# Kernel optimization log

Hardware: AMD Instinct MI355X
Metric: run time of the kernel (lower is better)

The kernel has to match this reference:

```python
import jax, jax.numpy as jnp
import numpy as np

B, CIN, CNECK, COUT = 8, 128, 128, 256
NV, NF = 10242, 20480  # icosphere level 5: nv = 10*4^5+2, nf = 20*4^5
EPS = 1e-5


def spmatmul(x, rows, cols, vals, m):
    # x: [..., N]; out[..., r] += vals[k] * x[..., cols[k]] for rows[k] == r
    g = x[..., cols] * vals
    return jnp.zeros(x.shape[:-1] + (m,), x.dtype).at[..., rows].add(g)


def conv1x1(x, w, b):
    # x: [B, Cin, N], w: [Cout, Cin], b: [Cout]
    return jnp.einsum('oi,bin->bon', w, x) + b[None, :, None]


def batchnorm1d(x, gamma, beta):
    # training-mode BN over (batch, spatial) per channel, biased variance
    mean = jnp.mean(x, axis=(0, 2), keepdims=True)
    var = jnp.var(x, axis=(0, 2), keepdims=True)
    xhat = (x - mean) * jax.lax.rsqrt(var + EPS)
    return gamma[None, :, None] * xhat + beta[None, :, None]


def setup_inputs() -> dict:
    key = jax.random.key(0)
    ks = jax.random.split(key, 16)

    def coo(k, nrows, per_row, ncols, scale):
        rows = jnp.repeat(jnp.arange(nrows, dtype=jnp.int32), per_row)
        cols = jax.random.randint(k, (nrows * per_row,), 0, ncols, dtype=jnp.int32)
        vals = jax.random.normal(jax.random.fold_in(k, 1), (nrows * per_row,), jnp.float32) * scale
        return rows, cols, vals

    Gr, Gc, Gv = coo(ks[0], 3 * NF, 3, NV, 0.5)
    Lr, Lc, Lv = coo(ks[1], NV, 7, NV, 0.3)
    Fr, Fc, Fv = coo(ks[2], NV, 6, NF, 1.0 / 6.0)

    def nrm(k, shape, scale=1.0):
        return jax.random.normal(k, shape, jnp.float32) * scale

    s_in = 1.0 / np.sqrt(CIN)
    s_nk = 1.0 / np.sqrt(CNECK)
    s_cf = 1.0 / np.sqrt(4 * CNECK)
    return {
        'x': nrm(ks[3], (B, CIN, NV)),
        'w1a': nrm(ks[4], (CNECK, CIN), s_in), 'b1a': nrm(ks[5], (CNECK,), s_in),
        'g1a': jnp.ones((CNECK,), jnp.float32), 'be1a': jnp.zeros((CNECK,), jnp.float32),
        'coeffs': nrm(ks[6], (CNECK * 4, CNECK), s_cf),
        'g2a': jnp.ones((CNECK,), jnp.float32), 'be2a': jnp.zeros((CNECK,), jnp.float32),
        'w3a': nrm(ks[7], (COUT, CNECK), s_nk), 'b3a': nrm(ks[8], (COUT,), s_nk),
        'g3a': jnp.ones((COUT,), jnp.float32), 'be3a': jnp.zeros((COUT,), jnp.float32),
        'w1b': nrm(ks[9], (COUT, CIN), s_in), 'b1b': nrm(ks[10], (COUT,), s_in),
        'g1b': jnp.ones((COUT,), jnp.float32), 'be1b': jnp.zeros((COUT,), jnp.float32),
        'G_vals': Gv, 'L_vals': Lv, 'F2V_vals': Fv,
        'EW': nrm(ks[11], (NF, 3)), 'NS': nrm(ks[12], (NF, 3)),
        'G_rows': Gr, 'G_cols': Gc,
        'L_rows': Lr, 'L_cols': Lc,
        'F2V_rows': Fr, 'F2V_cols': Fc,
    }


def mesh_conv(h, coeffs, G_rows, G_cols, G_vals, L_rows, L_cols, L_vals,
              F2V_rows, F2V_cols, F2V_vals, EW, NS):
    b, c, nv = h.shape
    # gradient on faces: [B,C,3*NF] -> [B,C,3,NF] -> [B,C,NF,3]
    grad_face = spmatmul(h, G_rows, G_cols, G_vals, 3 * NF)
    grad_face = grad_face.reshape(b, c, 3, NF).transpose(0, 1, 3, 2)
    laplacian = spmatmul(h, L_rows, L_cols, L_vals, NV)
    identity = h  # stride=1 => nv_prev == nv
    gf_ew = jnp.sum(grad_face * EW, axis=-1)  # [B,C,NF]
    gf_ns = jnp.sum(grad_face * NS, axis=-1)
    gv_ew = spmatmul(gf_ew, F2V_rows, F2V_cols, F2V_vals, NV)
    gv_ns = spmatmul(gf_ns, F2V_rows, F2V_cols, F2V_vals, NV)
    feat = jnp.stack([identity, laplacian, gv_ew, gv_ns], axis=-1)  # [B,C,NV,4]
    # [B,NV,C*4] @ [C*4,Cout] -> [B,Cout,NV]  (note: no bias added in original forward)
    out = jnp.matmul(feat.transpose(0, 2, 1, 3).reshape(b, nv, c * 4), coeffs)
    return out.transpose(0, 2, 1)


def reference(x, w1a, b1a, g1a, be1a, coeffs, g2a, be2a, w3a, b3a, g3a, be3a,
              w1b, b1b, g1b, be1b, G_vals, L_vals, F2V_vals, EW, NS,
              G_rows, G_cols, L_rows, L_cols, F2V_rows, F2V_cols):
    # shortcut branch: conv_1b -> bn_1b
    x2 = batchnorm1d(conv1x1(x, w1b, b1b), g1b, be1b)
    # main branch
    h = jax.nn.relu(batchnorm1d(conv1x1(x, w1a, b1a), g1a, be1a))
    h = mesh_conv(h, coeffs, G_rows, G_cols, G_vals, L_rows, L_cols, L_vals,
                  F2V_rows, F2V_cols, F2V_vals, EW, NS)
    h = jax.nn.relu(batchnorm1d(h, g2a, be2a))
    x1 = batchnorm1d(conv1x1(h, w3a, b3a), g3a, be3a)
    return jax.nn.relu(x1 + x2)
```

## Files before the change

### kernel.cpp

```cpp
#include <hip/hip_runtime.h>
#include <math.h>

#define BB   8
#define NVV  10242
#define NFF  20480
#define EPSBN 1e-5f
#define GRAM_BLOCKS 644

typedef __attribute__((ext_vector_type(8))) short bf16x8_t;
typedef __attribute__((ext_vector_type(4))) float f32x4_t;

__device__ inline float bf2f(ushort u) {
    union { uint i; float f; } v; v.i = ((uint)u) << 16; return v.f;
}
__device__ inline ushort f2bf(float f) {
    union { float f; uint i; } v; v.f = f;
    const uint r = v.i + 0x7fffu + ((v.i >> 16) & 1u);
    return (ushort)(r >> 16);
}
__device__ inline void unpack2(uint w, float& lo, float& hi) {
    union { uint i; float f; } a, b;
    a.i = w << 16; b.i = w & 0xffff0000u;
    lo = a.f; hi = b.f;
}
__device__ inline uint pack2(float lo, float hi) {
    return (uint)f2bf(lo) | ((uint)f2bf(hi) << 16);
}
__device__ inline void fma8(const uint4 hv, const float w, float s[8]) {
    float lo, hi;
    unpack2(hv.x, lo, hi); s[0] = fmaf(w, lo, s[0]); s[1] = fmaf(w, hi, s[1]);
    unpack2(hv.y, lo, hi); s[2] = fmaf(w, lo, s[2]); s[3] = fmaf(w, hi, s[3]);
    unpack2(hv.z, lo, hi); s[4] = fmaf(w, lo, s[4]); s[5] = fmaf(w, hi, s[5]);
    unpack2(hv.w, lo, hi); s[6] = fmaf(w, lo, s[6]); s[7] = fmaf(w, hi, s[7]);
}
__device__ inline uint4 pack8(const float s[8]) {
    uint4 p;
    p.x = pack2(s[0], s[1]); p.y = pack2(s[2], s[3]);
    p.z = pack2(s[4], s[5]); p.w = pack2(s[6], s[7]);
    return p;
}

__global__ __launch_bounds__(256)
void gram_kernel(const float* __restrict__ x, float* __restrict__ gramPart,
                 float* __restrict__ xsumPart, uint* __restrict__ xTu)
{
    __shared__ __align__(16) ushort Ahi[128 * 64];
    __shared__ __align__(16) ushort Alo[128 * 64];
    const int t = threadIdx.x;
    const int l = t & 63, wid = t >> 6;
    const int l15 = l & 15, l4 = l >> 4;
    f32x4_t acc[2][8];
#pragma unroll
    for (int m = 0; m < 2; ++m)
#pragma unroll
        for (int n = 0; n < 8; ++n) acc[m][n] = (f32x4_t){0.f, 0.f, 0.f, 0.f};
    float xs[8] = {0.f, 0.f, 0.f, 0.f, 0.f, 0.f, 0.f, 0.f};

    for (int s = 0; s < 2; ++s) {
        const int cc = blockIdx.x * 2 + s;
        const int b = cc / 161, tb = cc % 161, v0 = tb * 64;
#pragma unroll
        for (int i = 0; i < 8; ++i) {
            const int item = t + (i << 8);
            const int c = item >> 4, vq = item & 15;
            const int gv = v0 + (vq << 2);
            const float* xp = x + ((size_t)b * 128 + c) * NVV + gv;
            float4 xv = make_float4(0.f, 0.f, 0.f, 0.f);
            if (gv + 4 <= NVV) {
                xv = *reinterpret_cast<const float4*>(xp);
            } else {
                if (gv     < NVV) xv.x = xp[0];
                if (gv + 1 < NVV) xv.y = xp[1];
            }
            xs[i] += xv.x + xv.y + xv.z + xv.w;
            const ushort h0 = f2bf(xv.x), h1 = f2bf(xv.y), h2 = f2bf(xv.z), h3 = f2bf(xv.w);
            const ushort e0 = f2bf(xv.x - bf2f(h0)), e1 = f2bf(xv.y - bf2f(h1));
            const ushort e2 = f2bf(xv.z - bf2f(h2)), e3 = f2bf(xv.w - bf2f(h3));
            uint2 hp, lp;
            hp.x = (uint)h0 | ((uint)h1 << 16); hp.y = (uint)h2 | ((uint)h3 << 16);
            lp.x = (uint)e0 | ((uint)e1 << 16); lp.y = (uint)e2 | ((uint)e3 << 16);
            const int byte = (c << 7) + (vq << 3);
            const int swz = byte ^ ((c & 7) << 4);
            *reinterpret_cast<uint2*>((char*)Ahi + swz) = hp;
            *reinterpret_cast<uint2*>((char*)Alo + swz) = lp;
        }
        __syncthreads();
        {
            const int v = t & 63, cq = t >> 6;
            const int gv = v0 + v;
            if (gv < NVV) {
                uint4* rowp = reinterpret_cast<uint4*>(xTu + ((size_t)b * NVV + gv) * 64) + (cq << 2);
#pragma unroll
                for (int k2 = 0; k2 < 4; ++k2) {
                    uint wrd[4];
#pragma unroll
                    for (int w2 = 0; w2 < 4; ++w2) {
                        const int c0 = (cq << 5) + (k2 << 3) + (w2 << 1);
                        const int b0 = ((c0) << 7) + (v << 1);
                        const int b1 = ((c0 + 1) << 7) + (v << 1);
                        const ushort q0 = *reinterpret_cast<const ushort*>((const char*)Ahi + (b0 ^ ((c0 & 7) << 4)));
                        const ushort q1 = *reinterpret_cast<const ushort*>((const char*)Ahi + (b1 ^ (((c0 + 1) & 7) << 4)));
                        wrd[w2] = (uint)q0 | ((uint)q1 << 16);
                    }
                    rowp[k2] = make_uint4(wrd[0], wrd[1], wrd[2], wrd[3]);
                }
            }
        }
#pragma unroll
        for (int kk2 = 0; kk2 < 2; ++kk2) {
            bf16x8_t ah[2], al[2];
#pragma unroll
            for (int m = 0; m < 2; ++m) {
                const int row = wid * 32 + m * 16 + l15;
                const int byte = (row << 7) + (kk2 << 6) + (l4 << 4);
                ah[m] = *reinterpret_cast<const bf16x8_t*>((const char*)Ahi + (byte ^ ((row & 7) << 4)));
                al[m] = *reinterpret_cast<const bf16x8_t*>((const char*)Alo + (byte ^ ((row & 7) << 4)));
            }
#pragma unroll
            for (int n = 0; n < 8; ++n) {
                const int rn = n * 16 + l15;
                const int byte = (rn << 7) + (kk2 << 6) + (l4 << 4);
                const bf16x8_t bh = *reinterpret_cast<const bf16x8_t*>((const char*)Ahi + (byte ^ ((rn & 7) << 4)));
                const bf16x8_t bl = *reinterpret_cast<const bf16x8_t*>((const char*)Alo + (byte ^ ((rn & 7) << 4)));
#pragma unroll
                for (int m = 0; m < 2; ++m) {
                    acc[m][n] = __builtin_amdgcn_mfma_f32_16x16x32_bf16(ah[m], bh, acc[m][n], 0, 0, 0);
                    acc[m][n] = __builtin_amdgcn_mfma_f32_16x16x32_bf16(ah[m], bl, acc[m][n], 0, 0, 0);
                    acc[m][n] = __builtin_amdgcn_mfma_f32_16x16x32_bf16(al[m], bh, acc[m][n], 0, 0, 0);
                }
            }
        }
        __syncthreads();
    }
    float* gp = gramPart + (size_t)blockIdx.x * 16384;
#pragma unroll
    for (int m = 0; m < 2; ++m)
#pragma unroll
        for (int n = 0; n < 8; ++n)
#pragma unroll
            for (int j = 0; j < 4; ++j) {
                const int row = wid * 32 + m * 16 + l4 * 4 + j;
                const int col = n * 16 + l15;
                gp[row * 128 + col] = acc[m][n][j];
            }
#pragma unroll
    for (int i = 0; i < 8; ++i) {
        xs[i] += __shfl_xor(xs[i], 1);
        xs[i] += __shfl_xor(xs[i], 2);
        xs[i] += __shfl_xor(xs[i], 4);
        xs[i] += __shfl_xor(xs[i], 8);
    }
    if ((l & 15) == 0) {
#pragma unroll
        for (int i = 0; i < 8; ++i)
            xsumPart[(size_t)blockIdx.x * 128 + wid * 4 + l4 + i * 16] = xs[i];
    }
}

__global__ void reduce_gram_kernel(const float* __restrict__ gp, const float* __restrict__ xp,
                                   float* __restrict__ Gram, float* __restrict__ xsum)
{
    const int tid = blockIdx.x * 256 + threadIdx.x;
    for (int e = tid; e < 16384; e += 64 * 256) {
        float s = 0.f;
        for (int i = 0; i < GRAM_BLOCKS; ++i) s += gp[(size_t)i * 16384 + e];
        Gram[e] = s;
    }
    if (blockIdx.x == 0 && threadIdx.x < 128) {
        float s = 0.f;
        for (int i = 0; i < GRAM_BLOCKS; ++i) s += xp[(size_t)i * 128 + threadIdx.x];
        xsum[threadIdx.x] = s;
    }
}

__global__ __launch_bounds__(128)
void stats_ab_kernel(const float* __restrict__ Gram, const float* __restrict__ xsum,
                     const float* __restrict__ w1a, const float* __restrict__ g1a,
                     const float* __restrict__ be1a,
                     const float* __restrict__ w1b, const float* __restrict__ g1b,
                     const float* __restrict__ be1b,
                     float* __restrict__ alpha_a, float* __restrict__ beta_a,
                     float* __restrict__ alpha_b, float* __restrict__ beta_b)
{
    const int t = threadIdx.x;
    const int cc = blockIdx.x;
    const float invN = 1.f / (float)(BB * NVV);
    const bool isA = cc < 128;
    const int c = isA ? cc : cc - 128;
    const float* Wrow = isA ? (w1a + (size_t)c * 128) : (w1b + (size_t)c * 128);
    __shared__ float Wr[128];
    __shared__ float red[4];
    Wr[t] = Wrow[t];
    __syncthreads();
    float gi = 0.f;
    const float* Grow = Gram + (size_t)t * 128;
    for (int j = 0; j < 128; ++j) gi = fmaf(Grow[j], Wr[j], gi);
    float pi = Wr[t] * gi * invN;
    float qi = (xsum[t] * invN) * Wr[t];
    for (int off = 32; off > 0; off >>= 1) {
        pi += __shfl_down(pi, off);
        qi += __shfl_down(qi, off);
    }
    const int wid = t >> 6;
    if ((t & 63) == 0) { red[wid] = pi; red[2 + wid] = qi; }
    __syncthreads();
    if (t == 0) {
        const float P = red[0] + red[1], Q = red[2] + red[3];
        const float var = P - Q * Q;
        const float g = isA ? g1a[c] : g1b[c];
        const float be = isA ? be1a[c] : be1b[c];
        const float a = g * rsqrtf(var + EPSBN);
        if (isA) { alpha_a[c] = a; beta_a[c] = be - a * Q; }
        else     { alpha_b[c] = a; beta_b[c] = be - a * Q; }
    }
}

__global__ __launch_bounds__(256)
void prepack_weights_kernel(const float* __restrict__ w1a, const float* __restrict__ w1b,
                            const float* __restrict__ w3a, uint* __restrict__ wpk)
{
    const int j = blockIdx.x * 256 + threadIdx.x;
    const int seg = j >> 12;
    const int slab = seg >> 1, kc = (seg & 1) << 6;
    const int u = j & 4095;
    const int o = u >> 5;
    const int inner = (u << 2) & 127;
    const int inner0 = inner ^ ((o & 7) << 4);
    const int kp = inner0 >> 2;
    const float* W;
    if (slab == 0)      W = w1a;
    else if (slab <= 2) W = w1b + (size_t)(slab - 1) * 128 * 128;
    else                W = w3a + (size_t)(slab - 3) * 128 * 128;
    const float2 wv = *reinterpret_cast<const float2*>(&W[(size_t)o * 128 + kc + 2 * kp]);
    wpk[j] = pack2(wv.x, wv.y);
}

__global__ __launch_bounds__(256)
void prepack_coeffs_kernel(const float* __restrict__ coeffs, uint* __restrict__ cpk)
{
    const int j = blockIdx.x * 256 + threadIdx.x;
    const int chunk = j >> 12, u = j & 4095;
    const int o = u >> 5;
    const int inner = (u << 2) & 127;
    const int inner0 = inner ^ ((o & 7) << 4);
    const int p = inner0 >> 2;
    const int q = chunk >> 1, c0 = (chunk & 1) << 6;
    const int row0 = (c0 + 2 * p) * 4 + q;
    cpk[j] = pack2(coeffs[(size_t)row0 * 128 + o], coeffs[(size_t)(row0 + 4) * 128 + o]);
}

template <int MODE>
__global__ __launch_bounds__(256)
void mfma_conv_kernel(const ushort* __restrict__ Asrc, const uint4* __restrict__ wpk,
                      const float* __restrict__ aIn, const float* __restrict__ bIn,
                      const float* __restrict__ aA, const float* __restrict__ bA,
                      const float* __restrict__ aB, const float* __restrict__ bB,
                      ushort* __restrict__ hOut, ushort* __restrict__ x2Out,
                      ushort* __restrict__ x1Out,
                      float* __restrict__ statSum, float* __restrict__ statSsq)
{
    __shared__ __align__(16) ushort As[64 * 128];
    __shared__ __align__(16) ushort Bs[128 * 64];
    float* statS = (float*)Bs;
    float* statQ = (float*)Bs + 512;
    const int t = threadIdx.x;
    const int bid = blockIdx.x;
    const int b = bid & 7, vblk = bid >> 3;
    const int v0 = vblk * 64;
    const int l = t & 63, wid = t >> 6;
    const int l15 = l & 15, l4 = l >> 4;

#pragma unroll
    for (int i = 0; i < 4; ++i) {
        const int item = t + (i << 8);
        const int r = item >> 4, piece = item & 15;
        const int cb = piece * 8;
        const int v = v0 + r;
        uint4 pk = make_uint4(0u, 0u, 0u, 0u);
        if (v < NVV) {
            pk = *reinterpret_cast<const uint4*>(Asrc + ((size_t)b * NVV + v) * 128 + cb);
            if (MODE == 1) {
                float s[8];
                unpack2(pk.x, s[0], s[1]); unpack2(pk.y, s[2], s[3]);
                unpack2(pk.z, s[4], s[5]); unpack2(pk.w, s[6], s[7]);
                const float4 a0 = *reinterpret_cast<const float4*>(&aIn[cb]);
                const float4 a1 = *reinterpret_cast<const float4*>(&aIn[cb + 4]);
                const float4 b0 = *reinterpret_cast<const float4*>(&bIn[cb]);
                const float4 b1 = *reinterpret_cast<const float4*>(&bIn[cb + 4]);
                s[0] = fmaxf(fmaf(a0.x, s[0], b0.x), 0.f);
                s[1] = fmaxf(fmaf(a0.y, s[1], b0.y), 0.f);
                s[2] = fmaxf(fmaf(a0.z, s[2], b0.z), 0.f);
                s[3] = fmaxf(fmaf(a0.w, s[3], b0.w), 0.f);
                s[4] = fmaxf(fmaf(a1.x, s[4], b1.x), 0.f);
                s[5] = fmaxf(fmaf(a1.y, s[5], b1.y), 0.f);
                s[6] = fmaxf(fmaf(a1.z, s[6], b1.z), 0.f);
                s[7] = fmaxf(fmaf(a1.w, s[7], b1.w), 0.f);
                pk = pack8(s);
            }
        }
        const int byte = (r << 8) + (piece << 4);
        *reinterpret_cast<uint4*>((char*)As + (byte ^ ((r & 7) << 4))) = pk;
    }

    const int NZ = (MODE == 0) ? 3 : 2;
    for (int z = 0; z < NZ; ++z) {
        const int slab = (MODE == 0) ? z : (3 + z);
        f32x4_t acc[8];
#pragma unroll
        for (int n = 0; n < 8; ++n) acc[n] = (f32x4_t){0.f, 0.f, 0.f, 0.f};

        for (int kc = 0; kc < 128; kc += 64) {
            const uint4* wseg = wpk + (size_t)(slab * 2 + (kc >> 6)) * 1024;
#pragma unroll
            for (int i = 0; i < 4; ++i)
                reinterpret_cast<uint4*>(Bs)[t + (i << 8)] = wseg[t + (i << 8)];
            __syncthreads();
#pragma unroll
            for (int kk2 = 0; kk2 < 2; ++kk2) {
                const int row = wid * 16 + l15;
                const int abyte = (row << 8) + (kc << 1) + (kk2 << 6) + (l4 << 4);
                const bf16x8_t af = *reinterpret_cast<const bf16x8_t*>(
                    (const char*)As + (abyte ^ ((row & 7) << 4)));
#pragma unroll
                for (int n = 0; n < 8; ++n) {
                    const int o = n * 16 + l15;
                    const int bbyte = (o << 7) + (kk2 << 6) + (l4 << 4);
                    const bf16x8_t bfr = *reinterpret_cast<const bf16x8_t*>(
                        (const char*)Bs + (bbyte ^ ((o & 7) << 4)));
                    acc[n] = __builtin_amdgcn_mfma_f32_16x16x32_bf16(af, bfr, acc[n], 0, 0, 0);
                }
            }
            __syncthreads();
        }

        if (MODE == 0 && z == 0) {
            float aO[8], bO[8];
#pragma unroll
            for (int n = 0; n < 8; ++n) {
                const int c = n * 16 + l15;
                aO[n] = aA[c]; bO[n] = bA[c];
            }
#pragma unroll
            for (int j = 0; j < 4; ++j) {
                const int v = v0 + wid * 16 + l4 * 4 + j;
                if (v < NVV) {
                    ushort* mp = hOut + ((size_t)b * NVV + v) * 128 + l15;
#pragma unroll
                    for (int n = 0; n < 8; ++n)
                        mp[n * 16] = f2bf(fmaxf(fmaf(aO[n], acc[n][j], bO[n]), 0.f));
                }
            }
        } else if (MODE == 0) {
            float aO[8], bO[8];
#pragma unroll
            for (int n = 0; n < 8; ++n) {
                const int cl = n * 16 + l15;
                aO[n] = aB[(z - 1) * 128 + cl]; bO[n] = bB[(z - 1) * 128 + cl];
            }
            const int vbase = v0 + wid * 16 + l4 * 4;
#pragma unroll
            for (int n = 0; n < 8; ++n) {
                const int cl = n * 16 + l15;
                const int ch = (z - 1) * 128 + cl;
                ushort* p = x2Out + ((size_t)b * 256 + ch) * NVV + vbase;
                if (vbase + 4 <= NVV) {
                    uint* pu = (uint*)p;
                    pu[0] = pack2(fmaf(aO[n], acc[n][0], bO[n]),
                                  fmaf(aO[n], acc[n][1], bO[n]));
                    pu[1] = pack2(fmaf(aO[n], acc[n][2], bO[n]),
                                  fmaf(aO[n], acc[n][3], bO[n]));
                } else {
#pragma unroll
                    for (int j = 0; j < 4; ++j)
                        if (vbase + j < NVV)
                            p[j] = f2bf(fmaf(aO[n], acc[n][j], bO[n]));
                }
            }
        } else {
            float ss[8], sq[8];
#pragma unroll
            for (int n = 0; n < 8; ++n) { ss[n] = 0.f; sq[n] = 0.f; }
            const int vbase = v0 + wid * 16 + l4 * 4;
#pragma unroll
            for (int n = 0; n < 8; ++n) {
                const int cl = n * 16 + l15;
                const int ch = z * 128 + cl;
                ushort* p = x1Out + ((size_t)b * 256 + ch) * NVV + vbase;
                if (vbase + 4 <= NVV) {
                    float v0f = acc[n][0], v1f = acc[n][1];
                    float v2f = acc[n][2], v3f = acc[n][3];
                    uint* pu = (uint*)p;
                    pu[0] = pack2(v0f, v1f);
                    pu[1] = pack2(v2f, v3f);
                    ss[n] += v0f + v1f + v2f + v3f;
                    sq[n] = fmaf(v0f, v0f, sq[n]); sq[n] = fmaf(v1f, v1f, sq[n]);
                    sq[n] = fmaf(v2f, v2f, sq[n]); sq[n] = fmaf(v3f, v3f, sq[n]);
                } else {
#pragma unroll
                    for (int j = 0; j < 4; ++j) {
                        if (vbase + j < NVV) {
                            const float val = acc[n][j];
                            p[j] = f2bf(val);
                            ss[n] += val;
                            sq[n] = fmaf(val, val, sq[n]);
                        }
                    }
                }
            }
#pragma unroll
            for (int n = 0; n < 8; ++n) {
                ss[n] += __shfl_xor(ss[n], 16); ss[n] += __shfl_xor(ss[n], 32);
                sq[n] += __shfl_xor(sq[n], 16); sq[n] += __shfl_xor(sq[n], 32);
            }
            __syncthreads();
            if (l < 16) {
#pragma unroll
                for (int n = 0; n < 8; ++n) {
                    statS[wid * 128 + n * 16 + l] = ss[n];
                    statQ[wid * 128 + n * 16 + l] = sq[n];
                }
            }
            __syncthreads();
            if (t < 128) {
                const int slot = b * 161 + vblk;
                statSum[((size_t)z * 1288 + slot) * 128 + t] =
                    statS[t] + statS[128 + t] + statS[256 + t] + statS[384 + t];
                statSsq[((size_t)z * 1288 + slot) * 128 + t] =
                    statQ[t] + statQ[128 + t] + statQ[256 + t] + statQ[384 + t];
            }
            __syncthreads();
        }
    }
}

__global__ __launch_bounds__(256)
void face_kernel(const ushort* __restrict__ h, const float* __restrict__ Gv,
                 const int* __restrict__ Gc, const float* __restrict__ EW,
                 const float* __restrict__ NSm, ushort* __restrict__ gf)
{
    const int t = threadIdx.x;
    const int lane = t & 63, wid = t >> 6;
    const int bid = blockIdx.x;
    const int b = bid & 7;
    const int f = (bid >> 3) * 4 + wid;
    const uint* hb = (const uint*)h + (size_t)b * NVV * 64;
    float ewx = 0.f, ewy = 0.f, nsx = 0.f, nsy = 0.f;
#pragma unroll
    for (int e = 0; e < 3; ++e) {
        const size_t r3 = ((size_t)e * NFF + f) * 3;
        float gx = 0.f, gy = 0.f;
#pragma unroll
        for (int j = 0; j < 3; ++j) {
            const float w = Gv[r3 + j];
            const int col = Gc[r3 + j];
            const uint hv = hb[(size_t)col * 64 + lane];
            float lo, hi; unpack2(hv, lo, hi);
            gx = fmaf(w, lo, gx); gy = fmaf(w, hi, gy);
        }
        const float we = EW[f * 3 + e], wn = NSm[f * 3 + e];
        ewx = fmaf(we, gx, ewx); ewy = fmaf(we, gy, ewy);
        nsx = fmaf(wn, gx, nsx); nsy = fmaf(wn, gy, nsy);
    }
    uint* go = (uint*)gf + ((size_t)b * NFF + f) * 128;
    go[lane]      = pack2(ewx, ewy);
    go[64 + lane] = pack2(nsx, nsy);
}

__global__ __launch_bounds__(256, 8)
void mesh_gemm_kernel(const ushort* __restrict__ h, const ushort* __restrict__ gf,
                      const uint4* __restrict__ cpk,
                      const float* __restrict__ Lv, const int* __restrict__ Lc,
                      const float* __restrict__ Fv, const int* __restrict__ Fc,
                      ushort* __restrict__ meshraw,
                      float* __restrict__ msum, float* __restrict__ mssq)
{
    __shared__ __align__(16) ushort As[64 * 64];
    __shared__ __align__(16) ushort Bs[128 * 64];
    float* statS = (float*)Bs;
    float* statQ = (float*)Bs + 512;
    __shared__ int   LciS[448];
    __shared__ float LwS[448];
    __shared__ int   FciS[384];
    __shared__ float FwS[384];
    const int t = threadIdx.x;
    const int bid = blockIdx.x;
    const int b = bid & 7;
    const int vblk = bid >> 3;
    const int v0 = vblk * 64;
    const int l = t & 63, wid = t >> 6;
    const int l15 = l & 15, l4 = l >> 4;
    const size_t hb = (size_t)b * NVV * 128;

    for (int i = t; i < 448; i += 256) {
        const int g = v0 * 7 + i;
        if (g < NVV * 7) { LciS[i] = Lc[g]; LwS[i] = Lv[g]; }
    }
    for (int i = t; i < 384; i += 256) {
        const int g = v0 * 6 + i;
        if (g < NVV * 6) { FciS[i] = Fc[g]; FwS[i] = Fv[g]; }
    }
    __syncthreads();

    f32x4_t acc[8];
#pragma unroll
    for (int n = 0; n < 8; ++n) acc[n] = (f32x4_t){0.f, 0.f, 0.f, 0.f};

    for (int chunk = 0; chunk < 8; ++chunk) {
        const int q = chunk >> 1, c0 = (chunk & 1) << 6;
#pragma unroll
        for (int i = 0; i < 2; ++i) {
            const int item = t + (i << 8);
            const int r = item >> 3, piece = item & 7;
            const int cb = c0 + piece * 8;
            const int v = v0 + r;
            uint4 pk = make_uint4(0u, 0u, 0u, 0u);
            if (v < NVV) {
                if (q == 0) {
                    pk = *reinterpret_cast<const uint4*>(h + hb + (size_t)v * 128 + cb);
                } else if (q == 1) {
                    float s[8] = {0.f, 0.f, 0.f, 0.f, 0.f, 0.f, 0.f, 0.f};
#pragma unroll
                    for (int j = 0; j < 7; ++j) {
                        const float w = LwS[r * 7 + j];
                        const int col = LciS[r * 7 + j];
                        const uint4 hv = *reinterpret_cast<const uint4*>(h + hb + (size_t)col * 128 + cb);
                        fma8(hv, w, s);
                    }
                    pk = pack8(s);
                } else {
                    const int slab = q - 2;
                    float s[8] = {0.f, 0.f, 0.f, 0.f, 0.f, 0.f, 0.f, 0.f};
#pragma unroll
                    for (int j = 0; j < 6; ++j) {
                        const float w = FwS[r * 6 + j];
                        const int f = FciS[r * 6 + j];
                        const uint4 gv = *reinterpret_cast<const uint4*>(
                            gf + (((size_t)b * NFF + f) * 2 + slab) * 128 + cb);
                        fma8(gv, w, s);
                    }
                    pk = pack8(s);
                }
            }
            const int byte = (r << 7) + (piece << 4);
            *reinterpret_cast<uint4*>((char*)As + (byte ^ ((r & 7) << 4))) = pk;
        }
#pragma unroll
        for (int i = 0; i < 4; ++i) {
            const int idx = t + (i << 8);
            reinterpret_cast<uint4*>(Bs)[idx] = cpk[chunk * 1024 + idx];
        }
        __syncthreads();
#pragma unroll
        for (int kk2 = 0; kk2 < 2; ++kk2) {
            const int row = wid * 16 + l15;
            const int abyte = (row << 7) + (kk2 << 6) + (l4 << 4);
            const bf16x8_t af = *reinterpret_cast<const bf16x8_t*>(
                (const char*)As + (abyte ^ ((row & 7) << 4)));
#pragma unroll
            for (int n = 0; n < 8; ++n) {
                const int o = n * 16 + l15;
                const int bbyte = (o << 7) + (kk2 << 6) + (l4 << 4);
                const bf16x8_t bfr = *reinterpret_cast<const bf16x8_t*>(
                    (const char*)Bs + (bbyte ^ ((o & 7) << 4)));
                acc[n] = __builtin_amdgcn_mfma_f32_16x16x32_bf16(af, bfr, acc[n], 0, 0, 0);
            }
        }
        __syncthreads();
    }
    float ss[8], sq[8];
#pragma unroll
    for (int n = 0; n < 8; ++n) { ss[n] = 0.f; sq[n] = 0.f; }
#pragma unroll
    for (int j = 0; j < 4; ++j) {
        const int row = wid * 16 + l4 * 4 + j;
        const int v = v0 + row;
        if (v < NVV) {
            ushort* mp = meshraw + hb + (size_t)v * 128 + l15;
#pragma unroll
            for (int n = 0; n < 8; ++n) {
                const float val = acc[n][j];
                mp[n * 16] = f2bf(val);
                ss[n] += val;
                sq[n] = fmaf(val, val, sq[n]);
            }
        }
    }
#pragma unroll
    for (int n = 0; n < 8; ++n) {
        ss[n] += __shfl_xor(ss[n], 16); ss[n] += __shfl_xor(ss[n], 32);
        sq[n] += __shfl_xor(sq[n], 16); sq[n] += __shfl_xor(sq[n], 32);
    }
    if (l < 16) {
#pragma unroll
        for (int n = 0; n < 8; ++n) {
            statS[wid * 128 + n * 16 + l] = ss[n];
            statQ[wid * 128 + n * 16 + l] = sq[n];
        }
    }
    __syncthreads();
    if (t < 128) {
        const int blk = b * 161 + vblk;
        msum[(size_t)blk * 128 + t] = statS[t] + statS[128 + t] + statS[256 + t] + statS[384 + t];
        mssq[(size_t)blk * 128 + t] = statQ[t] + statQ[128 + t] + statQ[256 + t] + statQ[384 + t];
    }
}

__global__ __launch_bounds__(256)
void finalize_stats_kernel(const float* __restrict__ s, const float* __restrict__ q, int count,
                           const float* __restrict__ g, const float* __restrict__ be,
                           float* __restrict__ alpha, float* __restrict__ beta, int split)
{
    const int c = blockIdx.x, t = threadIdx.x;
    const size_t base = split ? ((size_t)(c >> 7) * count * 128 + (c & 127)) : (size_t)c;
    float ls = 0.f, lq = 0.f;
    for (int i = t; i < count; i += 256) {
        ls += s[base + (size_t)i * 128];
        lq += q[base + (size_t)i * 128];
    }
    __shared__ float rs[256], rq[256];
    rs[t] = ls; rq[t] = lq;
    __syncthreads();
    for (int off = 128; off > 0; off >>= 1) {
        if (t < off) { rs[t] += rs[t + off]; rq[t] += rq[t + off]; }
        __syncthreads();
    }
    if (t == 0) {
        const float invN = 1.f / (float)(BB * NVV);
        const float mean = rs[0] * invN;
        const float var = rq[0] * invN - mean * mean;
        const float a = g[c] * rsqrtf(var + EPSBN);
        alpha[c] = a;
        beta[c] = be[c] - a * mean;
    }
}

__global__ __launch_bounds__(256)
void final_kernel(float* __restrict__ out, const ushort* __restrict__ x1,
                  const ushort* __restrict__ x2,
                  const float* __restrict__ alpha3, const float* __restrict__ beta3)
{
    const int blk = blockIdx.x;
    const int o = blk & 255;
    const float a = alpha3[o], bb = beta3[o];
    float2* po = reinterpret_cast<float2*>(out + (size_t)blk * NVV);
    const uint* p1 = reinterpret_cast<const uint*>(x1 + (size_t)blk * NVV);
    const uint* p2 = reinterpret_cast<const uint*>(x2 + (size_t)blk * NVV);
    for (int i = threadIdx.x; i < NVV / 2; i += 256) {
        float a1, b1, a2, b2;
        unpack2(p1[i], a1, b1);
        unpack2(p2[i], a2, b2);
        po[i] = make_float2(fmaxf(fmaf(a, a1, bb) + a2, 0.f),
                            fmaxf(fmaf(a, b1, bb) + b2, 0.f));
    }
}

extern "C" void kernel_launch(void* const* d_in, const int* in_sizes, int n_in,
                              void* d_out, int out_size, void* d_ws, size_t ws_size,
                              hipStream_t stream)
{
    (void)in_sizes; (void)n_in; (void)out_size;
    const float* x      = (const float*)d_in[0];
    const float* w1a    = (const float*)d_in[1];
    const float* g1a    = (const float*)d_in[3];
    const float* be1a   = (const float*)d_in[4];
    const float* coeffs = (const float*)d_in[5];
    const float* g2a    = (const float*)d_in[6];
    const float* be2a   = (const float*)d_in[7];
    const float* w3a    = (const float*)d_in[8];
    const float* g3a    = (const float*)d_in[10];
    const float* be3a   = (const float*)d_in[11];
    const float* w1b    = (const float*)d_in[12];
    const float* g1b    = (const float*)d_in[14];
    const float* be1b   = (const float*)d_in[15];
    const float* Gv     = (const float*)d_in[16];
    const float* Lv     = (const float*)d_in[17];
    const float* Fv     = (const float*)d_in[18];
    const float* EW     = (const float*)d_in[19];
    const float* NSm    = (const float*)d_in[20];
    const int*   Gc     = (const int*)d_in[22];
    const int*   Lc     = (const int*)d_in[24];
    const int*   Fc     = (const int*)d_in[26];

    char* base = (char*)d_ws;
    size_t off = 0;
    auto alloc = [&](size_t bytes) { char* p = base + off; off += (bytes + 255) & ~(size_t)255; return p; };

    const size_t gfBytes = (size_t)BB * NFF * 2 * 128 * 2;
    char* region0   = alloc(gfBytes);
    float* gramPart = (float*)region0;
    float* xsumPart = (float*)(region0 + (size_t)GRAM_BLOCKS * 16384 * 4);
    ushort* gf      = (ushort*)region0;
    ushort* x1      = (ushort*)region0;

    ushort* xT      = (ushort*)alloc((size_t)BB * NVV * 128 * 2);
    ushort* h       = (ushort*)alloc((size_t)BB * NVV * 128 * 2);
    ushort* meshraw = (ushort*)alloc((size_t)BB * NVV * 128 * 2);
    ushort* x2      = (ushort*)alloc((size_t)BB * 256 * NVV * 2);
    uint*  cpk      = (uint*)alloc(32768 * 4);
    uint*  wpk      = (uint*)alloc(40960 * 4);
    float* Gram     = (float*)alloc(16384 * 4);
    float* xsum     = (float*)alloc(128 * 4);
    float* alpha_a  = (float*)alloc(128 * 4);
    float* beta_a   = (float*)alloc(128 * 4);
    float* alpha_b  = (float*)alloc(256 * 4);
    float* beta_b   = (float*)alloc(256 * 4);
    float* alpha2   = (float*)alloc(128 * 4);
    float* beta2    = (float*)alloc(128 * 4);
    float* alpha3   = (float*)alloc(256 * 4);
    float* beta3    = (float*)alloc(256 * 4);
    float* msum     = (float*)alloc((size_t)1288 * 128 * 4);
    float* mssq     = (float*)alloc((size_t)1288 * 128 * 4);
    float* x1sum    = (float*)alloc((size_t)2 * 1288 * 128 * 4);
    float* x1ssq    = (float*)alloc((size_t)2 * 1288 * 128 * 4);
    if (off > ws_size) return;

    gram_kernel<<<GRAM_BLOCKS, 256, 0, stream>>>(x, gramPart, xsumPart, (uint*)xT);
    reduce_gram_kernel<<<64, 256, 0, stream>>>(gramPart, xsumPart, Gram, xsum);
    stats_ab_kernel<<<384, 128, 0, stream>>>(Gram, xsum, w1a, g1a, be1a, w1b, g1b, be1b,
                                             alpha_a, beta_a, alpha_b, beta_b);
    prepack_coeffs_kernel<<<128, 256, 0, stream>>>(coeffs, cpk);
    prepack_weights_kernel<<<160, 256, 0, stream>>>(w1a, w1b, w3a, wpk);
    mfma_conv_kernel<0><<<1288, 256, 0, stream>>>(
        xT, (const uint4*)wpk, nullptr, nullptr, alpha_a, beta_a, alpha_b, beta_b,
        h, x2, nullptr, nullptr, nullptr);
    face_kernel<<<(NFF / 4) * 8, 256, 0, stream>>>(h, Gv, Gc, EW, NSm, gf);
    mesh_gemm_kernel<<<1288, 256, 0, stream>>>(h, gf, (const uint4*)cpk,
                                               Lv, Lc, Fv, Fc, meshraw, msum, mssq);
    finalize_stats_kernel<<<128, 256, 0, stream>>>(msum, mssq, 1288, g2a, be2a, alpha2, beta2, 0);
    mfma_conv_kernel<1><<<1288, 256, 0, stream>>>(
        meshraw, (const uint4*)wpk, alpha2, beta2, nullptr, nullptr, nullptr, nullptr,
        nullptr, nullptr, x1, x1sum, x1ssq);
    finalize_stats_kernel<<<256, 256, 0, stream>>>(x1sum, x1ssq, 1288, g3a, be3a, alpha3, beta3, 1);
    final_kernel<<<2048, 256, 0, stream>>>((float*)d_out, x1, x2, alpha3, beta3);
}
```

Baseline: 304.9 us.

## Apply gradient coefficients per face before F2V scatter to shrink mesh GEMM

Uses the linearity of the F2V sparse matmul to multiply the EW/NS face gradients by their coefficient slices per face with an MFMA GEMM. The result is a single 128-channel face tensor instead of two, so mesh_gemm_kernel gathers 6 chunks instead of 8 and reads half the face data. The added per-face GEMM runs over 20480 faces, about twice the vertex count. The mesh GEMM also gains identity-coefficient chunks that pass the face result through, and loses its occupancy launch bound.

```diff
diff --git a/kernel.cpp b/kernel.cpp
--- a/kernel.cpp
+++ b/kernel.cpp
@@ -32,6 +32,22 @@
     unpack2(hv.y, lo, hi); s[2] = fmaf(w, lo, s[2]); s[3] = fmaf(w, hi, s[3]);
     unpack2(hv.z, lo, hi); s[4] = fmaf(w, lo, s[4]); s[5] = fmaf(w, hi, s[5]);
     unpack2(hv.w, lo, hi); s[6] = fmaf(w, lo, s[6]); s[7] = fmaf(w, hi, s[7]);
+}
+__device__ inline void fma8x2(const uint4 hv, const float wa, const float wb,
+                              float sa[8], float sb[8]) {
+    float lo, hi;
+    unpack2(hv.x, lo, hi);
+    sa[0] = fmaf(wa, lo, sa[0]); sb[0] = fmaf(wb, lo, sb[0]);
+    sa[1] = fmaf(wa, hi, sa[1]); sb[1] = fmaf(wb, hi, sb[1]);
+    unpack2(hv.y, lo, hi);
+    sa[2] = fmaf(wa, lo, sa[2]); sb[2] = fmaf(wb, lo, sb[2]);
+    sa[3] = fmaf(wa, hi, sa[3]); sb[3] = fmaf(wb, hi, sb[3]);
+    unpack2(hv.z, lo, hi);
+    sa[4] = fmaf(wa, lo, sa[4]); sb[4] = fmaf(wb, lo, sb[4]);
+    sa[5] = fmaf(wa, hi, sa[5]); sb[5] = fmaf(wb, hi, sb[5]);
+    unpack2(hv.w, lo, hi);
+    sa[6] = fmaf(wa, lo, sa[6]); sb[6] = fmaf(wb, lo, sb[6]);
+    sa[7] = fmaf(wa, hi, sa[7]); sb[7] = fmaf(wb, hi, sb[7]);
 }
 __device__ inline uint4 pack8(const float s[8]) {
     uint4 p;
@@ -244,9 +260,25 @@
     const int inner = (u << 2) & 127;
     const int inner0 = inner ^ ((o & 7) << 4);
     const int p = inner0 >> 2;
-    const int q = chunk >> 1, c0 = (chunk & 1) << 6;
-    const int row0 = (c0 + 2 * p) * 4 + q;
-    cpk[j] = pack2(coeffs[(size_t)row0 * 128 + o], coeffs[(size_t)(row0 + 4) * 128 + o]);
+    float v0f, v1f;
+    if (chunk < 4) {
+        const int q = chunk >> 1, c0 = (chunk & 1) << 6;
+        const int row0 = (c0 + 2 * p) * 4 + q;
+        v0f = coeffs[(size_t)row0 * 128 + o];
+        v1f = coeffs[(size_t)(row0 + 4) * 128 + o];
+    } else if (chunk < 6) {
+        const int c0 = (chunk - 4) << 6;
+        v0f = (o == c0 + 2 * p) ? 1.f : 0.f;
+        v1f = (o == c0 + 2 * p + 1) ? 1.f : 0.f;
+    } else {
+        const int kc = chunk - 6;
+        const int kg0 = kc * 64 + 2 * p;
+        const int row0 = (kg0 < 128) ? (kg0 * 4 + 2) : ((kg0 - 128) * 4 + 3);
+        const int row1 = (kg0 + 1 < 128) ? ((kg0 + 1) * 4 + 2) : ((kg0 + 1 - 128) * 4 + 3);
+        v0f = coeffs[(size_t)row0 * 128 + o];
+        v1f = coeffs[(size_t)row1 * 128 + o];
+    }
+    cpk[j] = pack2(v0f, v1f);
 }
 
 template <int MODE>
@@ -434,40 +466,98 @@
 }
 
 __global__ __launch_bounds__(256)
-void face_kernel(const ushort* __restrict__ h, const float* __restrict__ Gv,
-                 const int* __restrict__ Gc, const float* __restrict__ EW,
-                 const float* __restrict__ NSm, ushort* __restrict__ gf)
-{
+void face_gemm_kernel(const ushort* __restrict__ h, const uint4* __restrict__ fBpk,
+                      const float* __restrict__ Gv, const int* __restrict__ Gc,
+                      const float* __restrict__ EW, const float* __restrict__ NSm,
+                      ushort* __restrict__ gface)
+{
+    __shared__ __align__(16) ushort Fg[4][64 * 64];
+    __shared__ __align__(16) ushort Bs[128 * 64];
+    __shared__ int   colS[576];
+    __shared__ float weS[576];
+    __shared__ float wnS[576];
     const int t = threadIdx.x;
-    const int lane = t & 63, wid = t >> 6;
     const int bid = blockIdx.x;
     const int b = bid & 7;
-    const int f = (bid >> 3) * 4 + wid;
-    const uint* hb = (const uint*)h + (size_t)b * NVV * 64;
-    float ewx = 0.f, ewy = 0.f, nsx = 0.f, nsy = 0.f;
-#pragma unroll
-    for (int e = 0; e < 3; ++e) {
-        const size_t r3 = ((size_t)e * NFF + f) * 3;
-        float gx = 0.f, gy = 0.f;
-#pragma unroll
-        for (int j = 0; j < 3; ++j) {
-            const float w = Gv[r3 + j];
-            const int col = Gc[r3 + j];
-            const uint hv = hb[(size_t)col * 64 + lane];
-            float lo, hi; unpack2(hv, lo, hi);
-            gx = fmaf(w, lo, gx); gy = fmaf(w, hi, gy);
-        }
-        const float we = EW[f * 3 + e], wn = NSm[f * 3 + e];
-        ewx = fmaf(we, gx, ewx); ewy = fmaf(we, gy, ewy);
-        nsx = fmaf(wn, gx, nsx); nsy = fmaf(wn, gy, nsy);
-    }
-    uint* go = (uint*)gf + ((size_t)b * NFF + f) * 128;
-    go[lane]      = pack2(ewx, ewy);
-    go[64 + lane] = pack2(nsx, nsy);
-}
-
-__global__ __launch_bounds__(256, 8)
-void mesh_gemm_kernel(const ushort* __restrict__ h, const ushort* __restrict__ gf,
+    const int f0 = (bid >> 3) * 64;
+    const int l = t & 63, wid = t >> 6;
+    const int l15 = l & 15, l4 = l >> 4;
+    const ushort* hb = h + (size_t)b * NVV * 128;
+
+    for (int i = t; i < 576; i += 256) {
+        const int r = i / 9, m = i - r * 9;
+        const int e = m / 3, jj = m - e * 3;
+        const int f = f0 + r;
+        const size_t gidx = ((size_t)e * NFF + f) * 3 + jj;
+        const float g = Gv[gidx];
+        colS[i] = Gc[gidx];
+        weS[i] = EW[f * 3 + e] * g;
+        wnS[i] = NSm[f * 3 + e] * g;
+    }
+    __syncthreads();
+
+#pragma unroll
+    for (int it = 0; it < 4; ++it) {
+        const int idx = t + (it << 8);
+        const int r = idx >> 4, p = idx & 15;
+        const int cb = p * 8;
+        float se[8] = {0.f, 0.f, 0.f, 0.f, 0.f, 0.f, 0.f, 0.f};
+        float sn[8] = {0.f, 0.f, 0.f, 0.f, 0.f, 0.f, 0.f, 0.f};
+#pragma unroll
+        for (int m = 0; m < 9; ++m) {
+            const int col = colS[r * 9 + m];
+            const uint4 hv = *reinterpret_cast<const uint4*>(hb + (size_t)col * 128 + cb);
+            fma8x2(hv, weS[r * 9 + m], wnS[r * 9 + m], se, sn);
+        }
+        const int ch = cb >> 6;
+        const int piece = (cb & 63) >> 3;
+        const int byte = (r << 7) + (piece << 4);
+        const int swz = byte ^ ((r & 7) << 4);
+        *reinterpret_cast<uint4*>((char*)Fg[ch] + swz)     = pack8(se);
+        *reinterpret_cast<uint4*>((char*)Fg[2 + ch] + swz) = pack8(sn);
+    }
+    __syncthreads();
+
+    f32x4_t acc[8];
+#pragma unroll
+    for (int n = 0; n < 8; ++n) acc[n] = (f32x4_t){0.f, 0.f, 0.f, 0.f};
+
+    for (int chunk = 0; chunk < 4; ++chunk) {
+#pragma unroll
+        for (int i = 0; i < 4; ++i)
+            reinterpret_cast<uint4*>(Bs)[t + (i << 8)] = fBpk[chunk * 1024 + t + (i << 8)];
+        __syncthreads();
+#pragma unroll
+        for (int kk2 = 0; kk2 < 2; ++kk2) {
+            const int row = wid * 16 + l15;
+            const int abyte = (row << 7) + (kk2 << 6) + (l4 << 4);
+            const bf16x8_t af = *reinterpret_cast<const bf16x8_t*>(
+                (const char*)Fg[chunk] + (abyte ^ ((row & 7) << 4)));
+#pragma unroll
+            for (int n = 0; n < 8; ++n) {
+                const int o = n * 16 + l15;
+                const int bbyte = (o << 7) + (kk2 << 6) + (l4 << 4);
+                const bf16x8_t bfr = *reinterpret_cast<const bf16x8_t*>(
+                    (const char*)Bs + (bbyte ^ ((o & 7) << 4)));
+                acc[n] = __builtin_amdgcn_mfma_f32_16x16x32_bf16(af, bfr, acc[n], 0, 0, 0);
+            }
+        }
+        __syncthreads();
+    }
+
+#pragma unroll
+    for (int j = 0; j < 4; ++j) {
+        const int r = wid * 16 + l4 * 4 + j;
+        const int f = f0 + r;
+        ushort* gp = gface + ((size_t)b * NFF + f) * 128 + l15;
+#pragma unroll
+        for (int n = 0; n < 8; ++n)
+            gp[n * 16] = f2bf(acc[n][j]);
+    }
+}
+
+__global__ __launch_bounds__(256)
+void mesh_gemm_kernel(const ushort* __restrict__ h, const ushort* __restrict__ gface,
                       const uint4* __restrict__ cpk,
                       const float* __restrict__ Lv, const int* __restrict__ Lc,
                       const float* __restrict__ Fv, const int* __restrict__ Fc,
@@ -505,7 +595,7 @@
 #pragma unroll
     for (int n = 0; n < 8; ++n) acc[n] = (f32x4_t){0.f, 0.f, 0.f, 0.f};
 
-    for (int chunk = 0; chunk < 8; ++chunk) {
+    for (int chunk = 0; chunk < 6; ++chunk) {
         const int q = chunk >> 1, c0 = (chunk & 1) << 6;
 #pragma unroll
         for (int i = 0; i < 2; ++i) {
@@ -528,14 +618,13 @@
                     }
                     pk = pack8(s);
                 } else {
-                    const int slab = q - 2;
                     float s[8] = {0.f, 0.f, 0.f, 0.f, 0.f, 0.f, 0.f, 0.f};
 #pragma unroll
                     for (int j = 0; j < 6; ++j) {
                         const float w = FwS[r * 6 + j];
                         const int f = FciS[r * 6 + j];
                         const uint4 gv = *reinterpret_cast<const uint4*>(
-                            gf + (((size_t)b * NFF + f) * 2 + slab) * 128 + cb);
+                            gface + ((size_t)b * NFF + f) * 128 + cb);
                         fma8(gv, w, s);
                     }
                     pk = pack8(s);
@@ -590,6 +679,7 @@
         ss[n] += __shfl_xor(ss[n], 16); ss[n] += __shfl_xor(ss[n], 32);
         sq[n] += __shfl_xor(sq[n], 16); sq[n] += __shfl_xor(sq[n], 32);
     }
+    __syncthreads();
     if (l < 16) {
 #pragma unroll
         for (int n = 0; n < 8; ++n) {
@@ -685,18 +775,18 @@
     size_t off = 0;
     auto alloc = [&](size_t bytes) { char* p = base + off; off += (bytes + 255) & ~(size_t)255; return p; };
 
-    const size_t gfBytes = (size_t)BB * NFF * 2 * 128 * 2;
-    char* region0   = alloc(gfBytes);
+    const size_t r0Bytes = (size_t)GRAM_BLOCKS * 16384 * 4 + (size_t)GRAM_BLOCKS * 128 * 4 + 4096;
+    char* region0   = alloc(r0Bytes);
     float* gramPart = (float*)region0;
     float* xsumPart = (float*)(region0 + (size_t)GRAM_BLOCKS * 16384 * 4);
-    ushort* gf      = (ushort*)region0;
+    ushort* gface   = (ushort*)region0;
     ushort* x1      = (ushort*)region0;
 
     ushort* xT      = (ushort*)alloc((size_t)BB * NVV * 128 * 2);
     ushort* h       = (ushort*)alloc((size_t)BB * NVV * 128 * 2);
     ushort* meshraw = (ushort*)alloc((size_t)BB * NVV * 128 * 2);
     ushort* x2      = (ushort*)alloc((size_t)BB * 256 * NVV * 2);
-    uint*  cpk      = (uint*)alloc(32768 * 4);
+    uint*  cpk      = (uint*)alloc(40960 * 4);
     uint*  wpk      = (uint*)alloc(40960 * 4);
     float* Gram     = (float*)alloc(16384 * 4);
     float* xsum     = (float*)alloc(128 * 4);
@@ -718,13 +808,14 @@
     reduce_gram_kernel<<<64, 256, 0, stream>>>(gramPart, xsumPart, Gram, xsum);
     stats_ab_kernel<<<384, 128, 0, stream>>>(Gram, xsum, w1a, g1a, be1a, w1b, g1b, be1b,
                                              alpha_a, beta_a, alpha_b, beta_b);
-    prepack_coeffs_kernel<<<128, 256, 0, stream>>>(coeffs, cpk);
+    prepack_coeffs_kernel<<<160, 256, 0, stream>>>(coeffs, cpk);
     prepack_weights_kernel<<<160, 256, 0, stream>>>(w1a, w1b, w3a, wpk);
     mfma_conv_kernel<0><<<1288, 256, 0, stream>>>(
         xT, (const uint4*)wpk, nullptr, nullptr, alpha_a, beta_a, alpha_b, beta_b,
         h, x2, nullptr, nullptr, nullptr);
-    face_kernel<<<(NFF / 4) * 8, 256, 0, stream>>>(h, Gv, Gc, EW, NSm, gf);
-    mesh_gemm_kernel<<<1288, 256, 0, stream>>>(h, gf, (const uint4*)cpk,
+    face_gemm_kernel<<<(NFF / 64) * 8, 256, 0, stream>>>(
+        h, (const uint4*)cpk + 6 * 1024, Gv, Gc, EW, NSm, gface);
+    mesh_gemm_kernel<<<1288, 256, 0, stream>>>(h, gface, (const uint4*)cpk,
                                                Lv, Lc, Fv, Fc, meshraw, msum, mssq);
     finalize_stats_kernel<<<128, 256, 0, stream>>>(msum, mssq, 1288, g2a, be2a, alpha2, beta2, 0);
     mfma_conv_kernel<1><<<1288, 256, 0, stream>>>(
```

Measured after the change: 275.7 us. 1.11x faster.
